# Performance work log

Hardware: AMD Instinct MI355X
Metric: run time of the kernel (lower is better)

Reference implementation:

```python
import jax, jax.numpy as jnp
import numpy as np

B, T, D, H, HS = 4, 1024, 1024, 16, 64  # T == block_size; HS = D // H


def setup_inputs() -> dict:
    key = jax.random.key(0)
    ks = jax.random.split(key, 9)
    s = 0.02
    x = jax.random.normal(ks[0], (B, T, D), dtype=jnp.float32)
    Wk = jax.random.normal(ks[1], (H, D, HS), dtype=jnp.float32) * s
    bk = jax.random.normal(ks[2], (H, HS), dtype=jnp.float32) * s
    Wq = jax.random.normal(ks[3], (H, D, HS), dtype=jnp.float32) * s
    bq = jax.random.normal(ks[4], (H, HS), dtype=jnp.float32) * s
    Wv = jax.random.normal(ks[5], (H, D, HS), dtype=jnp.float32) * s
    bv = jax.random.normal(ks[6], (H, HS), dtype=jnp.float32) * s
    Wp = jax.random.normal(ks[7], (D, D), dtype=jnp.float32) * s
    bp = jax.random.normal(ks[8], (D,), dtype=jnp.float32) * s
    return {"x": x, "Wk": Wk, "bk": bk, "Wq": Wq, "bq": bq,
            "Wv": Wv, "bv": bv, "Wp": Wp, "bp": bp}


def reference(x, Wk, bk, Wq, bq, Wv, bv, Wp, bp):
    Bx, Tx, Dx = x.shape
    # per-head projections, batched over heads: [B,H,T,HS]
    k = jnp.einsum('btd,hde->bhte', x, Wk) + bk[None, :, None, :]
    q = jnp.einsum('btd,hde->bhte', x, Wq) + bq[None, :, None, :]
    v = jnp.einsum('btd,hde->bhte', x, Wv) + bv[None, :, None, :]
    # NOTE: faithful to source: wei = k @ q^T, scaled by C**-0.5 with C=d_model
    scores = jnp.einsum('bhte,bhse->bhts', k, q) * (Dx ** -0.5)
    causal = jnp.tril(jnp.ones((Tx, Tx), dtype=bool))  # tril == 0 masked to -inf
    scores = jnp.where(causal[None, None], scores, -jnp.inf)
    attn = jax.nn.softmax(scores, axis=-1)  # attn_map (dropout is identity in eval)
    out = jnp.einsum('bhts,bhse->bhte', attn, v)
    # concat heads along feature dim (head order preserved)
    out = out.transpose(0, 2, 1, 3).reshape(Bx, Tx, -1)
    out = out @ Wp + bp  # final projection (output dropout identity in eval)
    return (out, attn)
```

## Files before the change

kernel.cpp:

```cpp
#include <hip/hip_runtime.h>
#include <hip/hip_bf16.h>
#include <stdint.h>


using f32x4 = __attribute__((ext_vector_type(4))) float;
using s16x8 = __attribute__((ext_vector_type(8))) short;

#define GLOAD_LDS16(g, l)                                                          \
  __builtin_amdgcn_global_load_lds((const __attribute__((address_space(1))) void*)(g), \
                                   (__attribute__((address_space(3))) void*)(l), 16, 0, 0)

__device__ __forceinline__ unsigned short f2bf(float f) {
  unsigned u = __float_as_uint(f);
  u = (u + 0x7FFFu + ((u >> 16) & 1u)) >> 16;
  return (unsigned short)u;
}

__global__ void prep_kernel(const float* __restrict__ x,
                            const float* __restrict__ Wk, const float* __restrict__ Wq,
                            const float* __restrict__ Wv,
                            const float* __restrict__ bk, const float* __restrict__ bq,
                            const float* __restrict__ bv,
                            const float* __restrict__ Wp,
                            unsigned short* __restrict__ xb,
                            unsigned short* __restrict__ Wt,
                            unsigned short* __restrict__ Wpt,
                            float* __restrict__ bqkv) {
  const int NX4 = 1048576;
  const int NW  = 3145728;
  const int NWP = 1048576;
  const int NB  = 3072;
  const int total = NX4 + NW + NWP + NB;
  for (int i = blockIdx.x * blockDim.x + threadIdx.x; i < total;
       i += gridDim.x * blockDim.x) {
    if (i < NX4) {
      float4 v = ((const float4*)x)[i];
      ushort4 o;
      o.x = f2bf(v.x); o.y = f2bf(v.y); o.z = f2bf(v.z); o.w = f2bf(v.w);
      ((ushort4*)xb)[i] = o;
    } else if (i < NX4 + NW) {
      int j = i - NX4;
      int n = j >> 10, d = j & 1023;
      int p = n >> 10, hc = n & 1023;
      int hh = hc >> 6, e = hc & 63;
      const float* Wsrc = (p == 0) ? Wk : (p == 1) ? Wq : Wv;
      Wt[(size_t)n * 1024 + d] = f2bf(Wsrc[((size_t)hh * 1024 + d) * 64 + e]);
    } else if (i < NX4 + NW + NWP) {
      int j = i - (NX4 + NW);
      int n = j >> 10, d = j & 1023;
      Wpt[(size_t)n * 1024 + d] = f2bf(Wp[(size_t)d * 1024 + n]);
    } else {
      int j = i - (NX4 + NW + NWP);
      int p = j >> 10, c = j & 1023;
      const float* bsrc = (p == 0) ? bk : (p == 1) ? bq : bv;
      bqkv[j] = bsrc[c];
    }
  }
}

template <int MODE>
__global__ __launch_bounds__(256, 2) void gemm_bt(
    const unsigned short* __restrict__ A,
    const unsigned short* __restrict__ Bt,
    const float* __restrict__ bias,
    unsigned short* __restrict__ kbuf,
    unsigned short* __restrict__ qbuf,
    unsigned short* __restrict__ vtbuf,
    float* __restrict__ fout,
    int gridN) {
  const int K = 1024;
  __shared__ __align__(16) unsigned short As[128 * 64];
  __shared__ __align__(16) unsigned short Bs[128 * 64];

  const int bm = blockIdx.x / gridN, bn = blockIdx.x % gridN;
  const int tid = threadIdx.x, wave = tid >> 6, lane = tid & 63;
  const int wm = wave >> 1, wn = wave & 1;
  const int l15 = lane & 15, l4 = lane >> 4;
  const long arow0 = (long)bm * 128;
  const long brow0 = (long)bn * 128;

  f32x4 acc[4][4];
  const f32x4 zf4 = {0.f, 0.f, 0.f, 0.f};
#pragma unroll
  for (int i = 0; i < 4; ++i)
#pragma unroll
    for (int j = 0; j < 4; ++j) acc[i][j] = zf4;

  for (int kt = 0; kt < 16; ++kt) {
#pragma unroll
    for (int s = 0; s < 4; ++s) {
      int ob = (wave * 4 + s) * 1024;
      int o = ob + lane * 16;
      int r = o >> 7;
      int cb = (o & 127) ^ ((r & 7) << 4);
      GLOAD_LDS16(A + (arow0 + r) * K + kt * 64 + (cb >> 1), (char*)As + ob);
      GLOAD_LDS16(Bt + (brow0 + r) * K + kt * 64 + (cb >> 1), (char*)Bs + ob);
    }
    __syncthreads();
#pragma unroll
    for (int kk = 0; kk < 2; ++kk) {
      s16x8 af[4], bfv[4];
#pragma unroll
      for (int i = 0; i < 4; ++i) {
        int row = wm * 64 + i * 16 + l15;
        int cb = (kk * 64 + l4 * 16) ^ ((row & 7) << 4);
        af[i] = *(const s16x8*)((const char*)As + row * 128 + cb);
      }
#pragma unroll
      for (int j = 0; j < 4; ++j) {
        int row = wn * 64 + j * 16 + l15;
        int cb = (kk * 64 + l4 * 16) ^ ((row & 7) << 4);
        bfv[j] = *(const s16x8*)((const char*)Bs + row * 128 + cb);
      }
#pragma unroll
      for (int i = 0; i < 4; ++i)
#pragma unroll
        for (int j = 0; j < 4; ++j)
          acc[i][j] = __builtin_amdgcn_mfma_f32_16x16x32_bf16(af[i], bfv[j], acc[i][j], 0, 0, 0);
    }
    __syncthreads();
  }

  const int gc0 = bn * 128;
  if (MODE == 0) {
    const int p = gc0 >> 10;
#pragma unroll
    for (int i = 0; i < 4; ++i) {
      int mrow = (int)arow0 + wm * 64 + i * 16 + l4 * 4;
      int b = mrow >> 10;
      int t = mrow & 1023;
#pragma unroll
      for (int j = 0; j < 4; ++j) {
        int gc = gc0 + wn * 64 + j * 16 + l15;
        int hc = gc & 1023;
        int hh = hc >> 6, e = hc & 63;
        float bb = bias[gc];
#pragma unroll
        for (int r = 0; r < 4; ++r) {
          unsigned short ub = f2bf(acc[i][j][r] + bb);
          if (p == 0)
            kbuf[(((long)(b * 16 + hh)) * 1024 + (t + r)) * 64 + e] = ub;
          else if (p == 1)
            qbuf[(((long)(b * 16 + hh)) * 1024 + (t + r)) * 64 + e] = ub;
          else
            vtbuf[(((long)(b * 16 + hh)) * 64 + e) * 1024 + (t + r)] = ub;
        }
      }
    }
  } else {
#pragma unroll
    for (int i = 0; i < 4; ++i) {
      long mrow = arow0 + wm * 64 + i * 16 + l4 * 4;
#pragma unroll
      for (int j = 0; j < 4; ++j) {
        int gc = gc0 + wn * 64 + j * 16 + l15;
        float bb = bias[gc];
#pragma unroll
        for (int r = 0; r < 4; ++r) fout[(mrow + r) * 1024 + gc] = acc[i][j][r] + bb;
      }
    }
  }
}

__global__ __launch_bounds__(256, 2) void attn_fused(
    const unsigned short* __restrict__ Kb,
    const unsigned short* __restrict__ Qb,
    const unsigned short* __restrict__ Vt,
    float* __restrict__ attn,
    unsigned short* __restrict__ outh) {
  __shared__ __align__(16) unsigned short Ps[128 * 128];
  __shared__ float rsum[2][128];
  __shared__ float rinv[128];

  const int bh = blockIdx.y;
  const int bx = blockIdx.x;
  const int ttile = (bx & 1) ? (7 - (bx >> 1)) : (bx >> 1);
  const int t0 = ttile * 128;
  const int b = bh >> 4, h = bh & 15;
  const unsigned short* Kbh = Kb + (long)bh * 65536;
  const unsigned short* Qbh = Qb + (long)bh * 65536;
  const unsigned short* Vbh = Vt + (long)bh * 65536;
  float* attn_bh = attn + (long)bh * 1048576;

  const int tid = threadIdx.x, wave = tid >> 6, lane = tid & 63;
  const int wm = wave >> 1, wn = wave & 1;
  const int l15 = lane & 15, l4 = lane >> 4;
  const f32x4 zf4 = {0.f, 0.f, 0.f, 0.f};

  s16x8 kf[4][2];
#pragma unroll
  for (int i = 0; i < 4; ++i)
#pragma unroll
    for (int kk = 0; kk < 2; ++kk)
      kf[i][kk] = *(const s16x8*)(Kbh + (long)(t0 + wm * 64 + i * 16 + l15) * 64 + kk * 32 + l4 * 8);

  float rs[4][4];
#pragma unroll
  for (int i = 0; i < 4; ++i)
#pragma unroll
    for (int r = 0; r < 4; ++r) rs[i][r] = 0.f;

  for (int st = 0; st <= ttile; ++st) {
    int s0 = st * 128;
    f32x4 acc[4][4];
#pragma unroll
    for (int i = 0; i < 4; ++i)
#pragma unroll
      for (int j = 0; j < 4; ++j) acc[i][j] = zf4;
#pragma unroll
    for (int kk = 0; kk < 2; ++kk) {
      s16x8 qf[4];
#pragma unroll
      for (int j = 0; j < 4; ++j)
        qf[j] = *(const s16x8*)(Qbh + (long)(s0 + wn * 64 + j * 16 + l15) * 64 + kk * 32 + l4 * 8);
#pragma unroll
      for (int i = 0; i < 4; ++i)
#pragma unroll
        for (int j = 0; j < 4; ++j)
          acc[i][j] = __builtin_amdgcn_mfma_f32_16x16x32_bf16(kf[i][kk], qf[j], acc[i][j], 0, 0, 0);
    }
    bool diag = (st == ttile);
#pragma unroll
    for (int i = 0; i < 4; ++i)
#pragma unroll
      for (int j = 0; j < 4; ++j)
#pragma unroll
        for (int r = 0; r < 4; ++r) {
          float sc = acc[i][j][r] * 0.03125f;
          if (diag) {
            int t = t0 + wm * 64 + i * 16 + l4 * 4 + r;
            int s = s0 + wn * 64 + j * 16 + l15;
            rs[i][r] += (s <= t) ? __expf(sc) : 0.f;
          } else {
            rs[i][r] += __expf(sc);
          }
        }
  }
#pragma unroll
  for (int i = 0; i < 4; ++i)
#pragma unroll
    for (int r = 0; r < 4; ++r) {
      float v = rs[i][r];
      v += __shfl_xor(v, 1);
      v += __shfl_xor(v, 2);
      v += __shfl_xor(v, 4);
      v += __shfl_xor(v, 8);
      if (l15 == 0) rsum[wn][wm * 64 + i * 16 + l4 * 4 + r] = v;
    }
  __syncthreads();
  if (tid < 128) rinv[tid] = 1.0f / (rsum[0][tid] + rsum[1][tid]);
  __syncthreads();

  float rinv_r[4][4];
#pragma unroll
  for (int i = 0; i < 4; ++i)
#pragma unroll
    for (int r = 0; r < 4; ++r) rinv_r[i][r] = rinv[wm * 64 + i * 16 + l4 * 4 + r];

  f32x4 acc2[2][4];
#pragma unroll
  for (int i = 0; i < 2; ++i)
#pragma unroll
    for (int j = 0; j < 4; ++j) acc2[i][j] = zf4;

  for (int st = 0; st < 8; ++st) {
    int s0 = st * 128;
    if (st > ttile) {
      float4 z = make_float4(0.f, 0.f, 0.f, 0.f);
#pragma unroll
      for (int q = 0; q < 16; ++q) {
        int fi = tid + q * 256;
        int row = fi >> 5, c4 = fi & 31;
        *(float4*)(attn_bh + (long)(t0 + row) * 1024 + s0 + c4 * 4) = z;
      }
      continue;
    }
    f32x4 acc[4][4];
#pragma unroll
    for (int i = 0; i < 4; ++i)
#pragma unroll
      for (int j = 0; j < 4; ++j) acc[i][j] = zf4;
#pragma unroll
    for (int kk = 0; kk < 2; ++kk) {
      s16x8 qf[4];
#pragma unroll
      for (int j = 0; j < 4; ++j)
        qf[j] = *(const s16x8*)(Qbh + (long)(s0 + wn * 64 + j * 16 + l15) * 64 + kk * 32 + l4 * 8);
#pragma unroll
      for (int i = 0; i < 4; ++i)
#pragma unroll
        for (int j = 0; j < 4; ++j)
          acc[i][j] = __builtin_amdgcn_mfma_f32_16x16x32_bf16(kf[i][kk], qf[j], acc[i][j], 0, 0, 0);
    }
    bool diag = (st == ttile);
#pragma unroll
    for (int i = 0; i < 4; ++i) {
      int tl = wm * 64 + i * 16 + l4 * 4;
#pragma unroll
      for (int j = 0; j < 4; ++j) {
        int sl = wn * 64 + j * 16 + l15;
#pragma unroll
        for (int r = 0; r < 4; ++r) {
          int t = t0 + tl + r;
          int s = s0 + sl;
          float p = (!diag || s <= t) ? __expf(acc[i][j][r] * 0.03125f) * rinv_r[i][r] : 0.f;
          attn_bh[(long)t * 1024 + s] = p;
          int lt = tl + r;
          Ps[lt * 128 + (sl ^ ((lt & 15) << 3))] = f2bf(p);
        }
      }
    }
    __syncthreads();
#pragma unroll
    for (int kk2 = 0; kk2 < 4; ++kk2) {
      s16x8 pf[2];
#pragma unroll
      for (int i2 = 0; i2 < 2; ++i2) {
        int lt = wave * 32 + i2 * 16 + l15;
        int ls = kk2 * 32 + l4 * 8;
        pf[i2] = *(const s16x8*)&Ps[lt * 128 + (ls ^ ((lt & 15) << 3))];
      }
      s16x8 vf[4];
#pragma unroll
      for (int j2 = 0; j2 < 4; ++j2)
        vf[j2] = *(const s16x8*)(Vbh + (long)(j2 * 16 + l15) * 1024 + s0 + kk2 * 32 + l4 * 8);
#pragma unroll
      for (int i2 = 0; i2 < 2; ++i2)
#pragma unroll
        for (int j2 = 0; j2 < 4; ++j2)
          acc2[i2][j2] = __builtin_amdgcn_mfma_f32_16x16x32_bf16(pf[i2], vf[j2], acc2[i2][j2], 0, 0, 0);
    }
    __syncthreads();
  }

#pragma unroll
  for (int i2 = 0; i2 < 2; ++i2)
#pragma unroll
    for (int j2 = 0; j2 < 4; ++j2)
#pragma unroll
      for (int r = 0; r < 4; ++r) {
        int t = t0 + wave * 32 + i2 * 16 + l4 * 4 + r;
        int e = j2 * 16 + l15;
        outh[(long)(b * 1024 + t) * 1024 + h * 64 + e] = f2bf(acc2[i2][j2][r]);
      }
}

extern "C" void kernel_launch(void* const* d_in, const int* in_sizes, int n_in,
                              void* d_out, int out_size, void* d_ws, size_t ws_size,
                              hipStream_t stream) {
  const float* x  = (const float*)d_in[0];
  const float* Wk = (const float*)d_in[1];
  const float* bk = (const float*)d_in[2];
  const float* Wq = (const float*)d_in[3];
  const float* bq = (const float*)d_in[4];
  const float* Wv = (const float*)d_in[5];
  const float* bv = (const float*)d_in[6];
  const float* Wp = (const float*)d_in[7];
  const float* bp = (const float*)d_in[8];

  char* ws = (char*)d_ws;
  unsigned short* xb   = (unsigned short*)(ws);
  unsigned short* Wt   = (unsigned short*)(ws + 8388608);
  unsigned short* Wpt  = (unsigned short*)(ws + 14680064);
  float*          bqkv = (float*)(ws + 16777216);
  unsigned short* Kbuf = (unsigned short*)(ws + 16789504);
  unsigned short* Qbuf = (unsigned short*)(ws + 25178112);
  unsigned short* Vtb  = (unsigned short*)(ws + 33566720);
  unsigned short* outh = (unsigned short*)(ws + 41955328);

  float* out  = (float*)d_out;
  float* attn = out + 4194304;

  prep_kernel<<<dim3(4096), dim3(256), 0, stream>>>(x, Wk, Wq, Wv, bk, bq, bv, Wp,
                                                    xb, Wt, Wpt, bqkv);
  gemm_bt<0><<<dim3(768), dim3(256), 0, stream>>>(xb, Wt, bqkv, Kbuf, Qbuf, Vtb,
                                                  (float*)nullptr, 24);
  attn_fused<<<dim3(8, 64), dim3(256), 0, stream>>>(Kbuf, Qbuf, Vtb, attn, outh);
  gemm_bt<1><<<dim3(256), dim3(256), 0, stream>>>(outh, Wpt, bp,
                                                  (unsigned short*)nullptr,
                                                  (unsigned short*)nullptr,
                                                  (unsigned short*)nullptr, out, 8);
}
```

Measured before the change: 530.7 us.

## Tile weight transposes through LDS and remap GEMM blocks across XCDs

Replaces the grid-stride prep kernel with a block-specialised kernel that transposes the QKV and projection weights through a padded 64x64 shared-memory tile, so both the global reads and the bf16 writes are coalesced instead of strided. It also remaps GEMM block indices so that consecutive tiles are assigned to the same XCD (blocks appear to be round-robined across 8 dies), improving L2 reuse of the A/B panels. The swizzle assumes the grid size is divisible by 8, which holds for 768 and 256.

```diff
diff --git a/kernel.cpp b/kernel.cpp
--- a/kernel.cpp
+++ b/kernel.cpp
@@ -16,44 +16,74 @@
   return (unsigned short)u;
 }
 
-__global__ void prep_kernel(const float* __restrict__ x,
-                            const float* __restrict__ Wk, const float* __restrict__ Wq,
-                            const float* __restrict__ Wv,
-                            const float* __restrict__ bk, const float* __restrict__ bq,
-                            const float* __restrict__ bv,
-                            const float* __restrict__ Wp,
-                            unsigned short* __restrict__ xb,
-                            unsigned short* __restrict__ Wt,
-                            unsigned short* __restrict__ Wpt,
-                            float* __restrict__ bqkv) {
-  const int NX4 = 1048576;
-  const int NW  = 3145728;
-  const int NWP = 1048576;
-  const int NB  = 3072;
-  const int total = NX4 + NW + NWP + NB;
-  for (int i = blockIdx.x * blockDim.x + threadIdx.x; i < total;
-       i += gridDim.x * blockDim.x) {
-    if (i < NX4) {
-      float4 v = ((const float4*)x)[i];
+__global__ __launch_bounds__(256) void prep2_kernel(
+    const float* __restrict__ x,
+    const float* __restrict__ Wk, const float* __restrict__ Wq,
+    const float* __restrict__ Wv,
+    const float* __restrict__ bk, const float* __restrict__ bq,
+    const float* __restrict__ bv,
+    const float* __restrict__ Wp,
+    unsigned short* __restrict__ xb,
+    unsigned short* __restrict__ Wt,
+    unsigned short* __restrict__ Wpt,
+    float* __restrict__ bqkv) {
+  __shared__ float tile[64][65];
+  const int bid = blockIdx.x, t = threadIdx.x;
+
+  if (bid < 1024) {
+#pragma unroll
+    for (int q = 0; q < 4; ++q) {
+      int idx = bid * 1024 + q * 256 + t;
+      float4 v = ((const float4*)x)[idx];
       ushort4 o;
       o.x = f2bf(v.x); o.y = f2bf(v.y); o.z = f2bf(v.z); o.w = f2bf(v.w);
-      ((ushort4*)xb)[i] = o;
-    } else if (i < NX4 + NW) {
-      int j = i - NX4;
-      int n = j >> 10, d = j & 1023;
-      int p = n >> 10, hc = n & 1023;
-      int hh = hc >> 6, e = hc & 63;
-      const float* Wsrc = (p == 0) ? Wk : (p == 1) ? Wq : Wv;
-      Wt[(size_t)n * 1024 + d] = f2bf(Wsrc[((size_t)hh * 1024 + d) * 64 + e]);
-    } else if (i < NX4 + NW + NWP) {
-      int j = i - (NX4 + NW);
-      int n = j >> 10, d = j & 1023;
-      Wpt[(size_t)n * 1024 + d] = f2bf(Wp[(size_t)d * 1024 + n]);
-    } else {
-      int j = i - (NX4 + NW + NWP);
-      int p = j >> 10, c = j & 1023;
+      ((ushort4*)xb)[idx] = o;
+    }
+  } else if (bid < 1792) {
+    int wb = bid - 1024;
+    int p = wb >> 8, rem = wb & 255;
+    int h = rem >> 4, dt = rem & 15;
+    int d0 = dt * 64;
+    const float* Wsrc = (p == 0) ? Wk : (p == 1) ? Wq : Wv;
+    const float* src = Wsrc + ((size_t)h * 1024 + d0) * 64;
+#pragma unroll
+    for (int q = 0; q < 16; ++q) {
+      int idx = t + q * 256;
+      int dr = idx >> 6, e = idx & 63;
+      tile[dr][e] = src[(size_t)dr * 64 + e];
+    }
+    __syncthreads();
+    unsigned short* dst = Wt + ((size_t)p * 1024 + h * 64) * 1024 + d0;
+#pragma unroll
+    for (int q = 0; q < 16; ++q) {
+      int idx = t + q * 256;
+      int er = idx >> 6, dc = idx & 63;
+      dst[(size_t)er * 1024 + dc] = f2bf(tile[dc][er]);
+    }
+  } else if (bid < 2048) {
+    int wb = bid - 1792;
+    int nt = wb >> 4, dt = wb & 15;
+    int n0 = nt * 64, d0 = dt * 64;
+#pragma unroll
+    for (int q = 0; q < 16; ++q) {
+      int idx = t + q * 256;
+      int dr = idx >> 6, nc = idx & 63;
+      tile[dr][nc] = Wp[(size_t)(d0 + dr) * 1024 + n0 + nc];
+    }
+    __syncthreads();
+#pragma unroll
+    for (int q = 0; q < 16; ++q) {
+      int idx = t + q * 256;
+      int er = idx >> 6, dc = idx & 63;
+      Wpt[(size_t)(n0 + er) * 1024 + d0 + dc] = f2bf(tile[dc][er]);
+    }
+  } else {
+#pragma unroll
+    for (int q = 0; q < 12; ++q) {
+      int c = q * 256 + t;
+      int p = c >> 10;
       const float* bsrc = (p == 0) ? bk : (p == 1) ? bq : bv;
-      bqkv[j] = bsrc[c];
+      bqkv[c] = bsrc[c & 1023];
     }
   }
 }
@@ -72,7 +102,9 @@
   __shared__ __align__(16) unsigned short As[128 * 64];
   __shared__ __align__(16) unsigned short Bs[128 * 64];
 
-  const int bm = blockIdx.x / gridN, bn = blockIdx.x % gridN;
+  const int cpx = gridDim.x >> 3;
+  const int bid2 = (blockIdx.x & 7) * cpx + (blockIdx.x >> 3);
+  const int bm = bid2 / gridN, bn = bid2 % gridN;
   const int tid = threadIdx.x, wave = tid >> 6, lane = tid & 63;
   const int wm = wave >> 1, wn = wave & 1;
   const int l15 = lane & 15, l4 = lane >> 4;
@@ -371,8 +403,8 @@
   float* out  = (float*)d_out;
   float* attn = out + 4194304;
 
-  prep_kernel<<<dim3(4096), dim3(256), 0, stream>>>(x, Wk, Wq, Wv, bk, bq, bv, Wp,
-                                                    xb, Wt, Wpt, bqkv);
+  prep2_kernel<<<dim3(2049), dim3(256), 0, stream>>>(x, Wk, Wq, Wv, bk, bq, bv, Wp,
+                                                     xb, Wt, Wpt, bqkv);
   gemm_bt<0><<<dim3(768), dim3(256), 0, stream>>>(xb, Wt, bqkv, Kbuf, Qbuf, Vtb,
                                                   (float*)nullptr, 24);
   attn_fused<<<dim3(8, 64), dim3(256), 0, stream>>>(Kbuf, Qbuf, Vtb, attn, outh);
```

After: 513.4 us. 3.3% less time.
